# Optimization experiments

Measured on AMD Instinct MI355X. Metric: run time of the kernel, lower is better.

## Reference

```python
import jax, jax.numpy as jnp
import numpy as np

B, C, HW, N, FS = 8, 1024, 14, 512, 14  # batch, channels, fmap size, num ROIs, feature_scal
SCALE = 1.0 / 16.0
IMG = 224.0


def setup_inputs() -> dict:
    key = jax.random.key(0)
    k1, k2, k3, k4 = jax.random.split(key, 4)
    tensor = jax.random.normal(k1, (B, C, HW, HW), dtype=jnp.float32)
    # ROI rows: [batch_idx, x1, y1, x2, y2] in 224-px image coords, guaranteed x2>x1, y2>y1
    bidx = jax.random.randint(k2, (N,), 0, B).astype(jnp.float32)
    xy1 = jax.random.uniform(k3, (N, 2), minval=0.0, maxval=100.0)
    wh = jax.random.uniform(k4, (N, 2), minval=16.0, maxval=124.0)
    xy2 = jnp.minimum(xy1 + wh, IMG)
    ROI = jnp.concatenate([bidx[:, None], xy1, xy2], axis=1)  # [N,5]
    return {"tensor": tensor, "ROI": ROI}


def _pool_matrix(start, end, fs):
    # Adaptive-avg-pool of slice [start:end] (length L) to fs bins, expressed as a
    # [N, fs(out bins), fs(input positions)] averaging matrix.
    L = end - start  # [N] ints, >= 1
    i = jnp.arange(fs)  # output bins
    b0 = (i[None, :] * L[:, None]) // fs                      # [N,fs] bin start (rel)
    b1 = ((i[None, :] + 1) * L[:, None] + fs - 1) // fs       # [N,fs] bin end (rel, excl)
    pos = jnp.arange(fs)[None, None, :] - start[:, None, None]  # [N,1,fs] rel input pos
    mask = (pos >= b0[:, :, None]) & (pos < b1[:, :, None])     # [N,fs,fs]
    cnt = jnp.maximum(b1 - b0, 1).astype(jnp.float32)
    return mask.astype(jnp.float32) / cnt[:, :, None]


def reference(tensor, ROI):
    fm_no = ROI[:, 0].astype(jnp.int32)          # which batch element per ROI
    coords = ROI[:, 1:] * SCALE                  # [N,4] = x1,y1,x2,y2 in fmap coords
    x1 = jnp.maximum(jnp.floor(coords[:, 0]), 0).astype(jnp.int32)
    y1 = jnp.maximum(jnp.floor(coords[:, 1]), 0).astype(jnp.int32)
    x2 = jnp.minimum(jnp.ceil(coords[:, 2]), FS).astype(jnp.int32)
    y2 = jnp.minimum(jnp.ceil(coords[:, 3]), FS).astype(jnp.int32)
    # torch code slices fm[:, :, x1:x2, y1:y2] -> x indexes rows (H), y indexes cols (W)
    Mr = _pool_matrix(x1, x2, FS)  # [N,14,14] row pooling
    Mc = _pool_matrix(y1, y2, FS)  # [N,14,14] col pooling
    fms = tensor[fm_no]            # [N,C,14,14] gather per-ROI feature map
    # pooled[n,c,i,j] = sum_{h,w} Mr[n,i,h] * fms[n,c,h,w] * Mc[n,j,w]
    return jnp.einsum('nih,nchw,njw->ncij', Mr, fms, Mc)
```

## Files before the change

kernel.cpp:

```cpp
#include <hip/hip_runtime.h>


#define FS_      14
#define PER_CH   196
#define C_       1024
#define CPB      32
#define QPC      49
#define NSTAGE4  (CPB * PER_CH / 4)
#define ACT      245

__global__ __launch_bounds__(256) void roi_pool_kernel(
    const float* __restrict__ tensor,
    const float* __restrict__ roi,
    float* __restrict__ out)
{
    __shared__ float s_plane[CPB * PER_CH];
    __shared__ alignas(16) int   s_o00[PER_CH], s_o01[PER_CH],
                                 s_o10[PER_CH], s_o11[PER_CH];
    __shared__ alignas(16) float s_mw[PER_CH], s_mh[PER_CH],
                                 s_mwh[PER_CH], s_inv[PER_CH];

    const unsigned bx = blockIdx.x;
    const unsigned n  = bx >> 5;
    const unsigned c0 = (bx & 31u) * CPB;

    const float* r = roi + n * 5;
    const int fm = (int)r[0];
    const int x1 = max((int)floorf(r[1] * 0.0625f), 0);
    const int y1 = max((int)floorf(r[2] * 0.0625f), 0);
    const int x2 = min((int)ceilf(r[3] * 0.0625f), FS_);
    const int y2 = min((int)ceilf(r[4] * 0.0625f), FS_);
    const unsigned Lh = (unsigned)(x2 - x1);
    const unsigned Lw = (unsigned)(y2 - y1);

    const unsigned tid = threadIdx.x;

    if (tid < PER_CH) {
        const unsigned p = tid;
        const unsigned i = p / 14u;
        const unsigned j = p - i * 14u;
        const unsigned h0 = (i * Lh) / 14u;
        const unsigned h1 = ((i + 1u) * Lh + 13u) / 14u;
        const unsigned w0 = (j * Lw) / 14u;
        const unsigned w1 = ((j + 1u) * Lw + 13u) / 14u;
        const int dh = (int)(h1 - h0) - 1;
        const int dw = (int)(w1 - w0) - 1;
        const int a00 = (x1 + (int)h0) * FS_ + (y1 + (int)w0);
        s_o00[p] = a00 * 4;
        s_o01[p] = (a00 + dw) * 4;
        s_o10[p] = (a00 + FS_ * dh) * 4;
        s_o11[p] = (a00 + FS_ * dh + dw) * 4;
        s_mw[p]  = (float)dw;
        s_mh[p]  = (float)dh;
        s_mwh[p] = (float)(dw & dh);
        const int cnt = (dh + 1) * (dw + 1);
        s_inv[p] = (cnt == 1) ? 1.0f : ((cnt == 2) ? 0.5f : 0.25f);
    }

    const float4* __restrict__ src4 =
        (const float4*)(tensor + ((size_t)fm * C_ + c0) * PER_CH);
    float4* __restrict__ dst4 = (float4*)s_plane;
#pragma unroll
    for (unsigned k = 0; k < 7; ++k) {
        unsigned fi = k * 256u + tid;
        if (fi < NSTAGE4) dst4[fi] = src4[fi];
    }

    __syncthreads();

    if (tid < ACT) {
        const unsigned tc = tid / QPC;
        const unsigned q  = tid - tc * QPC;

        const int4   O00 = ((const int4*)s_o00)[q];
        const int4   O01 = ((const int4*)s_o01)[q];
        const int4   O10 = ((const int4*)s_o10)[q];
        const int4   O11 = ((const int4*)s_o11)[q];
        const float4 MW  = ((const float4*)s_mw)[q];
        const float4 MH  = ((const float4*)s_mh)[q];
        const float4 MWH = ((const float4*)s_mwh)[q];
        const float4 INV = ((const float4*)s_inv)[q];

        float4* __restrict__ out4 =
            (float4*)(out + ((size_t)n * C_ + c0) * PER_CH);

#pragma unroll
        for (unsigned it = 0; it < 7; ++it) {
            const unsigned cl = it * 5u + tc;
            if (cl >= CPB) continue;
            const char* pb = (const char*)s_plane + cl * (PER_CH * 4);

            float4 o;
            {
                float v00 = *(const float*)(pb + O00.x);
                float v01 = *(const float*)(pb + O01.x);
                float v10 = *(const float*)(pb + O10.x);
                float v11 = *(const float*)(pb + O11.x);
                o.x = (v00 + MW.x * v01 + MH.x * v10 + MWH.x * v11) * INV.x;
            }
            {
                float v00 = *(const float*)(pb + O00.y);
                float v01 = *(const float*)(pb + O01.y);
                float v10 = *(const float*)(pb + O10.y);
                float v11 = *(const float*)(pb + O11.y);
                o.y = (v00 + MW.y * v01 + MH.y * v10 + MWH.y * v11) * INV.y;
            }
            {
                float v00 = *(const float*)(pb + O00.z);
                float v01 = *(const float*)(pb + O01.z);
                float v10 = *(const float*)(pb + O10.z);
                float v11 = *(const float*)(pb + O11.z);
                o.z = (v00 + MW.z * v01 + MH.z * v10 + MWH.z * v11) * INV.z;
            }
            {
                float v00 = *(const float*)(pb + O00.w);
                float v01 = *(const float*)(pb + O01.w);
                float v10 = *(const float*)(pb + O10.w);
                float v11 = *(const float*)(pb + O11.w);
                o.w = (v00 + MW.w * v01 + MH.w * v10 + MWH.w * v11) * INV.w;
            }

            out4[it * ACT + tid] = o;
        }
    }
}

extern "C" void kernel_launch(void* const* d_in, const int* in_sizes, int n_in,
                              void* d_out, int out_size, void* d_ws, size_t ws_size,
                              hipStream_t stream) {
    const float* tensor = (const float*)d_in[0];
    const float* roi    = (const float*)d_in[1];
    float* out = (float*)d_out;

    const int blocks = (out_size / (CPB * PER_CH));
    roi_pool_kernel<<<blocks, 256, 0, stream>>>(tensor, roi, out);
}
```

Measured before the change: 410.5 us.

## Stage ROI planes via global_load_lds and restructure pooling reads and stores

Replaces the register round-trip copy of the feature plane into LDS with the AMDGCN global_load_lds builtin when available. The pooling step now reads adjacent pairs from two base offsets, with a small zero pad at the end of the plane for safe over-reads, instead of four precomputed offsets plus a mask. Outputs are written as strided scalar stores rather than float4 stores. This cuts LDS metadata and VGPR traffic during staging, but may reduce store coalescing width, and the builtin path's 16-byte size support depends on the target.

```diff
diff --git a/kernel.cpp b/kernel.cpp
--- a/kernel.cpp
+++ b/kernel.cpp
@@ -9,16 +9,20 @@
 #define NSTAGE4  (CPB * PER_CH / 4)
 #define ACT      245
 
+#if defined(__has_builtin)
+# if __has_builtin(__builtin_amdgcn_global_load_lds)
+#  define USE_GLL 1
+# endif
+#endif
+
 __global__ __launch_bounds__(256) void roi_pool_kernel(
     const float* __restrict__ tensor,
     const float* __restrict__ roi,
     float* __restrict__ out)
 {
-    __shared__ float s_plane[CPB * PER_CH];
-    __shared__ alignas(16) int   s_o00[PER_CH], s_o01[PER_CH],
-                                 s_o10[PER_CH], s_o11[PER_CH];
-    __shared__ alignas(16) float s_mw[PER_CH], s_mh[PER_CH],
-                                 s_mwh[PER_CH], s_inv[PER_CH];
+    __shared__ float s_plane[CPB * PER_CH + 4];
+    __shared__ alignas(16) int   s_o00[PER_CH], s_o10[PER_CH];
+    __shared__ alignas(16) float s_mw[PER_CH], s_mh[PER_CH], s_inv[PER_CH];
 
     const unsigned bx = blockIdx.x;
     const unsigned n  = bx >> 5;
@@ -47,14 +51,13 @@
         const int dw = (int)(w1 - w0) - 1;
         const int a00 = (x1 + (int)h0) * FS_ + (y1 + (int)w0);
         s_o00[p] = a00 * 4;
-        s_o01[p] = (a00 + dw) * 4;
         s_o10[p] = (a00 + FS_ * dh) * 4;
-        s_o11[p] = (a00 + FS_ * dh + dw) * 4;
         s_mw[p]  = (float)dw;
         s_mh[p]  = (float)dh;
-        s_mwh[p] = (float)(dw & dh);
         const int cnt = (dh + 1) * (dw + 1);
         s_inv[p] = (cnt == 1) ? 1.0f : ((cnt == 2) ? 0.5f : 0.25f);
+    } else if (tid < PER_CH + 4u) {
+        s_plane[CPB * PER_CH + (tid - PER_CH)] = 0.0f;
     }
 
     const float4* __restrict__ src4 =
@@ -63,7 +66,16 @@
 #pragma unroll
     for (unsigned k = 0; k < 7; ++k) {
         unsigned fi = k * 256u + tid;
-        if (fi < NSTAGE4) dst4[fi] = src4[fi];
+        if (fi < NSTAGE4) {
+#if defined(USE_GLL)
+            __builtin_amdgcn_global_load_lds(
+                (const __attribute__((address_space(1))) void*)(src4 + fi),
+                (__attribute__((address_space(3))) void*)(dst4 + fi),
+                16, 0, 0);
+#else
+            dst4[fi] = src4[fi];
+#endif
+        }
     }
 
     __syncthreads();
@@ -72,55 +84,39 @@
         const unsigned tc = tid / QPC;
         const unsigned q  = tid - tc * QPC;
 
-        const int4   O00 = ((const int4*)s_o00)[q];
-        const int4   O01 = ((const int4*)s_o01)[q];
-        const int4   O10 = ((const int4*)s_o10)[q];
-        const int4   O11 = ((const int4*)s_o11)[q];
-        const float4 MW  = ((const float4*)s_mw)[q];
-        const float4 MH  = ((const float4*)s_mh)[q];
-        const float4 MWH = ((const float4*)s_mwh)[q];
-        const float4 INV = ((const float4*)s_inv)[q];
+        int   O00[4], O10[4];
+        float MW[4], MH[4], INV[4];
+#pragma unroll
+        for (int k = 0; k < 4; ++k) {
+            const unsigned p = q + QPC * (unsigned)k;
+            O00[k] = s_o00[p];
+            O10[k] = s_o10[p];
+            MW[k]  = s_mw[p];
+            MH[k]  = s_mh[p];
+            INV[k] = s_inv[p];
+        }
 
-        float4* __restrict__ out4 =
-            (float4*)(out + ((size_t)n * C_ + c0) * PER_CH);
+        float* __restrict__ ob =
+            out + ((size_t)n * C_ + c0) * PER_CH + q;
 
 #pragma unroll
         for (unsigned it = 0; it < 7; ++it) {
             const unsigned cl = it * 5u + tc;
             if (cl >= CPB) continue;
             const char* pb = (const char*)s_plane + cl * (PER_CH * 4);
+            float* __restrict__ op = ob + cl * PER_CH;
 
-            float4 o;
-            {
-                float v00 = *(const float*)(pb + O00.x);
-                float v01 = *(const float*)(pb + O01.x);
-                float v10 = *(const float*)(pb + O10.x);
-                float v11 = *(const float*)(pb + O11.x);
-                o.x = (v00 + MW.x * v01 + MH.x * v10 + MWH.x * v11) * INV.x;
+#pragma unroll
+            for (int k = 0; k < 4; ++k) {
+                const char* p0 = pb + O00[k];
+                const float v00 = *(const float*)(p0);
+                const float v01 = *(const float*)(p0 + 4);
+                const char* p1 = pb + O10[k];
+                const float v10 = *(const float*)(p1);
+                const float v11 = *(const float*)(p1 + 4);
+                const float s = fmaf(MW[k], v01, v00) + MH[k] * fmaf(MW[k], v11, v10);
+                op[k * QPC] = s * INV[k];
             }
-            {
-                float v00 = *(const float*)(pb + O00.y);
-                float v01 = *(const float*)(pb + O01.y);
-                float v10 = *(const float*)(pb + O10.y);
-                float v11 = *(const float*)(pb + O11.y);
-                o.y = (v00 + MW.y * v01 + MH.y * v10 + MWH.y * v11) * INV.y;
-            }
-            {
-                float v00 = *(const float*)(pb + O00.z);
-                float v01 = *(const float*)(pb + O01.z);
-                float v10 = *(const float*)(pb + O10.z);
-                float v11 = *(const float*)(pb + O11.z);
-                o.z = (v00 + MW.z * v01 + MH.z * v10 + MWH.z * v11) * INV.z;
-            }
-            {
-                float v00 = *(const float*)(pb + O00.w);
-                float v01 = *(const float*)(pb + O01.w);
-                float v10 = *(const float*)(pb + O10.w);
-                float v11 = *(const float*)(pb + O11.w);
-                o.w = (v00 + MW.w * v01 + MH.w * v10 + MWH.w * v11) * INV.w;
-            }
-
-            out4[it * ACT + tid] = o;
         }
     }
 }
```

Result: no change. 413.8 us (+0.8%).
